# Kernel optimization log

Measured on AMD Instinct MI355X. Metric: run time of the kernel, lower is better.

Reference implementation:

```python
import jax, jax.numpy as jnp
import numpy as np

MAX_LENGTH = 400
NULL_TERM_IND = 52
THR = 1.0 - 1e-05  # F.threshold threshold value


def leaky(x):
    # F.leaky_relu default negative_slope=0.01
    return jnp.where(x >= 0, x, 0.01 * x)


def gru_cell(x, h, w_ih, w_hh, b_ih, b_hh):
    # torch.nn.GRUCell math
    gi = x @ w_ih.T + b_ih          # [B, 3H]
    gh = h @ w_hh.T + b_hh          # [B, 3H]
    i_r, i_z, i_n = jnp.split(gi, 3, axis=-1)
    h_r, h_z, h_n = jnp.split(gh, 3, axis=-1)
    r = jax.nn.sigmoid(i_r + h_r)
    z = jax.nn.sigmoid(i_z + h_z)
    n = jnp.tanh(i_n + r * h_n)
    return (1.0 - z) * n + z * h


def setup_inputs() -> dict:
    key = jax.random.key(0)
    ks = jax.random.split(key, 9)
    B, D, H, C = 2048, 4096, 128, 96
    def init(k, shape, fan):
        return (jax.random.uniform(k, shape, jnp.float32) * 2.0 - 1.0) / np.sqrt(fan)
    return {
        "img_feat": jax.random.normal(ks[0], (B, D), jnp.float32),
        "lin1_w": init(ks[1], (H, D), D),
        "lin1_b": init(ks[2], (H,), D),
        "w_ih": init(ks[3], (3 * H, H), H),
        "w_hh": init(ks[4], (3 * H, H), H),
        "b_ih": init(ks[5], (3 * H,), H),
        "b_hh": init(ks[6], (3 * H,), H),
        "lin2_w": init(ks[7], (C, H), H),
        "lin2_b": init(ks[8], (C,), H),
    }


def reference(img_feat, lin1_w, lin1_b, w_ih, w_hh, b_ih, b_hh, lin2_w, lin2_b):
    # ht: GRU input at t=0 is leaky_relu(lin1(img_feat)); hidden starts at zeros.
    ht = leaky(img_feat @ lin1_w.T + lin1_b)   # [B, 128]
    h0 = jnp.zeros_like(ht)

    def step(carry, _):
        ht, h0 = carry
        hn = gru_cell(ht, h0, w_ih, w_hh, b_ih, b_hh)
        # original: ht = char_gen(ht, h0); h0 = ht -> input == hidden next step
        chars = leaky(hn) @ lin2_w.T + lin2_b   # [B, C]
        m = jax.lax.stop_gradient(jnp.max(chars, axis=-1, keepdims=True))  # .data detach
        cn = chars / m
        cn = jnp.where(cn > THR, cn, 0.0)       # F.threshold(x, 1-1e-5, 0)
        return (hn, hn), cn

    _, titles = jax.lax.scan(step, (ht, h0), None, length=MAX_LENGTH)  # [T, B, C]
    titles = jnp.transpose(titles, (1, 0, 2))   # [B, T, C]

    # title_lens: first t with titles[b, t, NULL_TERM_IND] == 1, else MAX_LENGTH
    eq = titles[:, :, NULL_TERM_IND] == 1.0     # [B, T]
    first = jnp.argmax(eq, axis=1)
    lens = jnp.where(eq.any(axis=1), first + 1, MAX_LENGTH).astype(jnp.int32)
    return titles, lens
```

## Files before the change

### kernel.cpp

```cpp
#include <hip/hip_runtime.h>
#include <math.h>

#define NB   8
#define TT   400
#define HH   128
#define CC   96
#define DD   4096
#define THRV (1.0f - 1e-5f)
#define XR   40
#define HEPS 4e-6f
#define S10  1024.0f
#define IS10 0.0009765625f
#define IS20 9.5367431640625e-07f
#define SCW  132
#define SCS  1056

typedef _Float16 f16x8 __attribute__((ext_vector_type(8)));
typedef float    f32x4 __attribute__((ext_vector_type(4)));
typedef float    f32x2 __attribute__((ext_vector_type(2)));
typedef int      i32x4 __attribute__((ext_vector_type(4)));
typedef unsigned long long ull;

__device__ __forceinline__ float rcp_fast(float x) {
#if __has_builtin(__builtin_amdgcn_rcpf)
    return __builtin_amdgcn_rcpf(x);
#else
    return 1.0f / x;
#endif
}
__device__ __forceinline__ float sigm(float v)  { return rcp_fast(1.0f + __expf(-v)); }
__device__ __forceinline__ float ftanh(float x) { return 1.0f - 2.0f * rcp_fast(1.0f + __expf(2.0f * x)); }

__device__ __forceinline__ void split2(float4 u0, float4 u1, f16x8& hi, f16x8& lo) {
    float x[8] = {u0.x, u0.y, u0.z, u0.w, u1.x, u1.y, u1.z, u1.w};
    #pragma unroll
    for (int e = 0; e < 8; ++e) {
        _Float16 h = (_Float16)x[e];
        hi[e] = h;
        lo[e] = (_Float16)(x[e] - (float)h);
    }
}
__device__ __forceinline__ void split2s(float4 u0, float4 u1, f16x8& hi, f16x8& lo) {
    float x[8] = {u0.x, u0.y, u0.z, u0.w, u1.x, u1.y, u1.z, u1.w};
    #pragma unroll
    for (int e = 0; e < 8; ++e) {
        _Float16 h = (_Float16)x[e];
        hi[e] = h;
        lo[e] = (_Float16)((x[e] - (float)h) * S10);
    }
}
__device__ __forceinline__ void split1(float x, _Float16& hi, _Float16& lo) {
    hi = (_Float16)x;
    lo = (_Float16)(x - (float)hi);
}

__device__ __forceinline__ float xsum32(float v) {
#if __has_builtin(__builtin_amdgcn_permlane32_swap)
    auto r = __builtin_amdgcn_permlane32_swap(__float_as_uint(v), __float_as_uint(v), false, false);
    return __uint_as_float(r[0]) + __uint_as_float(r[1]);
#else
    return v + __shfl_xor(v, 32, 64);
#endif
}

__device__ __forceinline__ void step_barrier() {
    __builtin_amdgcn_sched_barrier(0);
    asm volatile("s_waitcnt lgkmcnt(0)" ::: "memory");
    __builtin_amdgcn_s_barrier();
    asm volatile("" ::: "memory");
    __builtin_amdgcn_sched_barrier(0);
}

__global__ __launch_bounds__(1024, 4)
void gru_title(const float* __restrict__ img,
               const float* __restrict__ l1w,
               const float* __restrict__ l1b,
               const float* __restrict__ wih,
               const float* __restrict__ whh,
               const float* __restrict__ bih,
               const float* __restrict__ bhh,
               const float* __restrict__ l2w,
               const float* __restrict__ l2b,
               float* __restrict__ out,
               float* __restrict__ lens)
{
    __shared__ alignas(16) _Float16 x2 [2][64][XR];
    __shared__ alignas(16) _Float16 l2v[2][64][XR];
    __shared__ alignas(16) char     x2i8[2][64][32];
    __shared__ alignas(16) _Float16 bcS[2][6][4][4][16][8];
    __shared__ alignas(16) float    gEx[4096];
    __shared__ alignas(16) float    scr[2 * SCS];
    __shared__ alignas(16) float    xs0[NB][HH];
    __shared__ int sh_st[4];

    const int tid  = threadIdx.x;
    const int b0   = blockIdx.x * NB;
    const int w    = tid >> 6;
    const int lane = tid & 63;
    const int lm   = lane & 15;
    const int lq   = lane >> 4;
    const int c8   = w & 7;
    const int r8   = w >> 3;
    const int ic2  = 16 * c8 + lm;

    f16x8 bh[2][4];
    i32x4 bq[2][2];
    float gb[2], fq[2];
    #pragma unroll
    for (int gl = 0; gl < 2; ++gl) {
        const int g2 = 2 * r8 + gl;
        const float* r0;
        const float* r1 = nullptr;
        float bsum;
        if (g2 == 0)      { r0 = wih + (size_t)ic2 * HH;         r1 = whh + (size_t)ic2 * HH;         bsum = bih[ic2] + bhh[ic2]; }
        else if (g2 == 1) { r0 = wih + (size_t)(128 + ic2) * HH; r1 = whh + (size_t)(128 + ic2) * HH; bsum = bih[128 + ic2] + bhh[128 + ic2]; }
        else if (g2 == 2) { r0 = wih + (size_t)(256 + ic2) * HH;                                      bsum = bih[256 + ic2]; }
        else              { r0 = whh + (size_t)(256 + ic2) * HH;                                      bsum = bhh[256 + ic2]; }
        gb[gl] = bsum;
        float bl32[4][8];
        #pragma unroll
        for (int kt = 0; kt < 4; ++kt) {
            const int k0 = 32 * kt + 8 * lq;
            float4 u0 = *(const float4*)(r0 + k0);
            float4 u1 = *(const float4*)(r0 + k0 + 4);
            if (r1) {
                float4 e0 = *(const float4*)(r1 + k0);
                float4 e1 = *(const float4*)(r1 + k0 + 4);
                u0.x += e0.x; u0.y += e0.y; u0.z += e0.z; u0.w += e0.w;
                u1.x += e1.x; u1.y += e1.y; u1.z += e1.z; u1.w += e1.w;
            }
            float xv[8] = {u0.x, u0.y, u0.z, u0.w, u1.x, u1.y, u1.z, u1.w};
            f16x8 hiv;
            #pragma unroll
            for (int e = 0; e < 8; ++e) {
                _Float16 hh = (_Float16)xv[e];
                hiv[e] = hh;
                bl32[kt][e] = xv[e] - (float)hh;
            }
            bh[gl][kt] = hiv;
        }
        float mx = 0.f;
        #pragma unroll
        for (int kt = 0; kt < 4; ++kt)
            #pragma unroll
            for (int e = 0; e < 8; ++e) mx = fmaxf(mx, fabsf(bl32[kt][e]));
        mx = fmaxf(mx, __shfl_xor(mx, 16, 64));
        mx = fmaxf(mx, __shfl_xor(mx, 32, 64));
        const float inv = (mx > 0.f) ? 127.0f / mx : 0.f;
        fq[gl] = mx * (1.0f / 16129.0f);
        ull p[4];
        #pragma unroll
        for (int kt = 0; kt < 4; ++kt) {
            ull pv = 0;
            #pragma unroll
            for (int e = 0; e < 8; ++e) {
                int q = (int)rintf(bl32[kt][e] * inv);
                pv |= ((ull)((unsigned)q & 0xffu)) << (8 * e);
            }
            p[kt] = pv;
        }
        #pragma unroll
        for (int ktp = 0; ktp < 2; ++ktp) {
            ull s0a = __shfl(p[2 * ktp],     lm + 16 * ((2 * lq) & 3), 64);
            ull s0b = __shfl(p[2 * ktp + 1], lm + 16 * ((2 * lq) & 3), 64);
            ull lo8 = (lq & 2) ? s0b : s0a;
            ull s1a = __shfl(p[2 * ktp],     lm + 16 * ((2 * lq + 1) & 3), 64);
            ull s1b = __shfl(p[2 * ktp + 1], lm + 16 * ((2 * lq + 1) & 3), 64);
            ull hi8 = (lq & 2) ? s1b : s1a;
            i32x4 f;
            f[0] = (int)(unsigned)(lo8 & 0xffffffffu);
            f[1] = (int)(unsigned)(lo8 >> 32);
            f[2] = (int)(unsigned)(hi8 & 0xffffffffu);
            f[3] = (int)(unsigned)(hi8 >> 32);
            bq[gl][ktp] = f;
        }
    }

    const int ct = (w >= 1 && w <= 6) ? (w - 1) : -1;
    float cb = 0.f;
    if (ct >= 0) cb = l2b[16 * ct + lm];

    for (int idx = tid; idx < 6 * 4 * 4 * 16; idx += 1024) {
        int t_  = idx;
        int lm_ = t_ & 15; t_ >>= 4;
        int lq_ = t_ & 3;  t_ >>= 2;
        int kt_ = t_ & 3;  t_ >>= 2;
        int ct_ = t_;
        const int n  = 16 * ct_ + lm_;
        const int k0 = 32 * kt_ + 8 * lq_;
        #pragma unroll
        for (int e = 0; e < 8; ++e) {
            float v = l2w[(size_t)n * HH + k0 + e];
            _Float16 hi = (_Float16)v;
            bcS[0][ct_][kt_][lq_][lm_][e] = hi;
            bcS[1][ct_][kt_][lq_][lm_][e] = (_Float16)(v - (float)hi);
        }
    }

    if (tid < 4) sh_st[tid] = 1;
    ((int*)x2i8)[tid] = 0;

    {
        const int m8 = lm & 7;
        const float* arow = img + (size_t)(b0 + m8) * DD + 8 * lq + 2048 * r8;
        const float* brow = l1w + (size_t)ic2 * DD + 8 * lq + 2048 * r8;
        f32x4 z4 = {0.f, 0.f, 0.f, 0.f};
        f32x4 accP0 = z4, accP1 = z4, accQ0 = z4, accQ1 = z4;
        auto ptile = [&](int kt, f32x4& aP, f32x4& aQ) {
            float4 a0  = *(const float4*)(arow + 32 * kt);
            float4 a1  = *(const float4*)(arow + 32 * kt + 4);
            float4 bb0 = *(const float4*)(brow + 32 * kt);
            float4 bb1 = *(const float4*)(brow + 32 * kt + 4);
            f16x8 ah, al, bhf, blf;
            split2s(a0, a1, ah, al);
            split2s(bb0, bb1, bhf, blf);
            f16x8 af = (lm >= 8) ? al : ah;
            aP = __builtin_amdgcn_mfma_f32_16x16x32_f16(af, bhf, aP, 0, 0, 0);
            aQ = __builtin_amdgcn_mfma_f32_16x16x32_f16(af, blf, aQ, 0, 0, 0);
        };
        #pragma unroll 2
        for (int kt = 0; kt < 64; kt += 2) {
            ptile(kt,     accP0, accQ0);
            ptile(kt + 1, accP1, accQ1);
        }
        f32x4 P = accP0 + accP1;
        f32x4 Q = accQ0 + accQ1;
        const float sP = (lane < 32) ? 1.0f : IS10;
        const float sQ = (lane < 32) ? IS10 : IS20;
        float s0 = xsum32(P[0] * sP + Q[0] * sQ);
        float s1 = xsum32(P[1] * sP + Q[1] * sQ);
        float s2 = xsum32(P[2] * sP + Q[2] * sQ);
        float s3 = xsum32(P[3] * sP + Q[3] * sQ);
        if (lane < 32) {
            float vv[4] = {s0, s1, s2, s3};
            #pragma unroll
            for (int reg = 0; reg < 4; ++reg)
                scr[r8 * SCS + (4 * lq + reg) * SCW + ic2] = vv[reg];
        }
    }
    __syncthreads();
    {
        const int m = tid >> 7, c = tid & 127;
        float v = scr[m * SCW + c] + scr[SCS + m * SCW + c] + l1b[c];
        xs0[m][c] = (v >= 0.f) ? v : 0.01f * v;
    }
    __syncthreads();

    const int mA = (lane < 32) ? 4 * lq : 4 * (lq - 2) + 2;

    const int mB  = w >> 1;
    const int iB  = 64 * (w & 1) + lane;
    const int kWr = (iB >> 3) & 3;
    const int rBq = 16 * kWr;
    const int cS  = 8 * (((iB >> 5) & 3) ^ kWr) + (iB & 7);
    const int r8q = 16 * ((iB >> 4) & 3) + mB;
    const int c8q = 16 * (iB >> 6) + (iB & 15);
    const unsigned gRd = (unsigned)(mB * 2048 + iB * 16) ^ ((unsigned)(mB & 3) << 5);

    float hreg = 0.f;
    int  len   = TT;
    bool found = false;
    int  tex   = TT;

    auto chars_mfma = [&](int slot, f32x4& cA, f32x4& cB) {
        #pragma unroll
        for (int kt = 0; kt < 4; ++kt) {
            f16x8 cf = *(const f16x8*)&l2v[slot][lane][8 * (kt ^ lq)];
            f16x8 bH = *(const f16x8*)&bcS[0][ct][kt][lq][lm][0];
            f16x8 bL = *(const f16x8*)&bcS[1][ct][kt][lq][lm][0];
            f32x4& a = (kt < 2) ? cA : cB;
            a = __builtin_amdgcn_mfma_f32_16x16x32_f16(cf, bH, a, 0, 0, 0);
            a = __builtin_amdgcn_mfma_f32_16x16x32_f16(cf, bL, a, 0, 0, 0);
        }
    };
    auto chars_commit = [&](int slot, f32x4 cA, f32x4 cB) {
        f32x4 ca = cA + cB;
        const int n = 16 * ct + lm;
        float s0 = xsum32(ca[0]);
        float s1 = xsum32(ca[1]);
        float s2 = xsum32(ca[2]);
        float s3 = xsum32(ca[3]);
        scr[slot * SCS + mA * SCW + n]       = ((lane < 32) ? s0 : s2) + cb;
        scr[slot * SCS + (mA + 1) * SCW + n] = ((lane < 32) ? s1 : s3) + cb;
    };

    auto outrow = [&](int slot, int tme, int r) {
        const float* cr = &scr[slot * SCS + r * SCW];
        float a0 = cr[lane];
        float a1 = cr[32 + lane];
        float a2 = cr[64 + lane];
        float mx = fmaxf(fmaxf(a0, a1), a2);
        mx = fmaxf(mx, __shfl_xor(mx, 16, 32));
        mx = fmaxf(mx, __shfl_xor(mx, 8, 32));
        mx = fmaxf(mx, __shfl_xor(mx, 4, 32));
        mx = fmaxf(mx, __shfl_xor(mx, 2, 32));
        mx = fmaxf(mx, __shfl_xor(mx, 1, 32));
        float q0 = a0 / mx;
        float q1 = a1 / mx;
        float q2 = a2 / mx;
        if (lane < 32) {
            size_t base = ((size_t)(b0 + r) * TT + tme) * CC;
            out[base + lane]      = (q0 > THRV) ? q0 : 0.f;
            out[base + 32 + lane] = (q1 > THRV) ? q1 : 0.f;
            out[base + 64 + lane] = (q2 > THRV) ? q2 : 0.f;
        }
        float q52 = __shfl(q1, 20, 64);
        if (!found && q52 == 1.0f) { found = true; len = tme + 1; }
    };

    for (int t = 0; t < TT; ++t) {
        const int pr = (t + 1) & 1;
        const int pc = t & 1;

        if (t == 0) {
            if (tid < 512) {
                const int g = tid >> 7;
                const int i = tid & 127;
                float bsum;
                if (g == 0)      bsum = bih[i] + bhh[i];
                else if (g == 1) bsum = bih[128 + i] + bhh[128 + i];
                else if (g == 2) bsum = bih[256 + i];
                else             bsum = bhh[256 + i];
                float accT[NB];
                #pragma unroll
                for (int m = 0; m < NB; ++m) accT[m] = bsum;
                if (g < 3) {
                    const float4* wp = (const float4*)(wih + (size_t)(128 * g + i) * HH);
                    #pragma unroll
                    for (int k = 0; k < HH / 4; ++k) {
                        float4 wv = wp[k];
                        #pragma unroll
                        for (int m = 0; m < NB; ++m) {
                            float4 x = *(const float4*)&xs0[m][4 * k];
                            accT[m] += wv.x * x.x + wv.y * x.y + wv.z * x.z + wv.w * x.w;
                        }
                    }
                }
                #pragma unroll
                for (int m = 0; m < NB; ++m) {
                    unsigned off = (unsigned)(m * 2048 + i * 16 + g * 4) ^ ((unsigned)(m & 3) << 5);
                    *(float*)((char*)gEx + off) = accT[m];
                }
            }
        } else {
            f32x4 z4 = {0.f, 0.f, 0.f, 0.f};
            i32x4 iz = {0, 0, 0, 0};
            if (ct >= 0) {
                f32x4 cc0 = z4, cc1 = z4;
                chars_mfma(pr, cc0, cc1);
                chars_commit(pr, cc0, cc1);
            }
            f32x4 acc[2] = {z4, z4};
            i32x4 qac[2] = {iz, iz};
            {
                f16x8 afA = *(const f16x8*)&x2[pr][lane][8 * (0 ^ lq)];
                f16x8 afB = *(const f16x8*)&x2[pr][lane][8 * (1 ^ lq)];
                acc[0] = __builtin_amdgcn_mfma_f32_16x16x32_f16(afA, bh[0][0], acc[0], 0, 0, 0);
                acc[1] = __builtin_amdgcn_mfma_f32_16x16x32_f16(afA, bh[1][0], acc[1], 0, 0, 0);
                acc[0] = __builtin_amdgcn_mfma_f32_16x16x32_f16(afB, bh[0][1], acc[0], 0, 0, 0);
                acc[1] = __builtin_amdgcn_mfma_f32_16x16x32_f16(afB, bh[1][1], acc[1], 0, 0, 0);
                afA = *(const f16x8*)&x2[pr][lane][8 * (2 ^ lq)];
                afB = *(const f16x8*)&x2[pr][lane][8 * (3 ^ lq)];
                acc[0] = __builtin_amdgcn_mfma_f32_16x16x32_f16(afA, bh[0][2], acc[0], 0, 0, 0);
                acc[1] = __builtin_amdgcn_mfma_f32_16x16x32_f16(afA, bh[1][2], acc[1], 0, 0, 0);
                acc[0] = __builtin_amdgcn_mfma_f32_16x16x32_f16(afB, bh[0][3], acc[0], 0, 0, 0);
                acc[1] = __builtin_amdgcn_mfma_f32_16x16x32_f16(afB, bh[1][3], acc[1], 0, 0, 0);
                i32x4 ia = *(const i32x4*)&x2i8[pr][lane][0];
                qac[0] = __builtin_amdgcn_mfma_i32_16x16x64_i8(ia, bq[0][0], qac[0], 0, 0, 0);
                qac[1] = __builtin_amdgcn_mfma_i32_16x16x64_i8(ia, bq[1][0], qac[1], 0, 0, 0);
                ia = *(const i32x4*)&x2i8[pr][lane][16];
                qac[0] = __builtin_amdgcn_mfma_i32_16x16x64_i8(ia, bq[0][1], qac[0], 0, 0, 0);
                qac[1] = __builtin_amdgcn_mfma_i32_16x16x64_i8(ia, bq[1][1], qac[1], 0, 0, 0);
            }
            float G[2][2];
            #pragma unroll
            for (int gl = 0; gl < 2; ++gl) {
                f32x4 t4;
                #pragma unroll
                for (int rr = 0; rr < 4; ++rr)
                    t4[rr] = acc[gl][rr] + fq[gl] * (float)qac[gl][rr];
                float c0 = xsum32(t4[0]);
                float c1 = xsum32(t4[1]);
                float c2 = xsum32(t4[2]);
                float c3 = xsum32(t4[3]);
                G[gl][0] = ((lane < 32) ? c0 : c2) + gb[gl];
                G[gl][1] = ((lane < 32) ? c1 : c3) + gb[gl];
            }
            #pragma unroll
            for (int s = 0; s < 2; ++s) {
                const int m = mA + s;
                unsigned off = (unsigned)(m * 2048 + ic2 * 16 + r8 * 8) ^ ((unsigned)(m & 3) << 5);
                f32x2 v2 = {G[0][s], G[1][s]};
                *(f32x2*)((char*)gEx + off) = v2;
            }
            if (w >= 8 && t >= 2) outrow(pc, t - 2, w - 8);
        }
        step_barrier();

        {
            float4 g4 = *(const float4*)((const char*)gEx + gRd);
            float r = sigm(g4.x);
            float z = sigm(g4.y);
            float n = ftanh(g4.z + r * g4.w);
            float hp = (t == 0) ? 0.f : hreg;
            float h  = (1.f - z) * n + z * hp;
            bool chg = (t < 2) | (fabsf(h - hp) > HEPS);
            hreg = h;
            float lv = (h >= 0.f) ? h : 0.01f * h;
            _Float16 a, b;
            split1(h, a, b);
            x2[pc][rBq + mB][cS]     = a;
            x2[pc][rBq + 8 + mB][cS] = b;
            split1(lv, a, b);
            l2v[pc][rBq + mB][cS]     = a;
            l2v[pc][rBq + 8 + mB][cS] = b;
            x2i8[pc][r8q][c8q] = (char)(int)rintf(h * 127.0f);
            if (chg) sh_st[t & 3] = 0;
        }
        if (tid == 0) sh_st[(t + 2) & 3] = 1;
        step_barrier();
        if (t >= 2 && sh_st[t & 3]) { tex = t; break; }
    }

    if (tex == TT) {
        const int pl = (TT - 1) & 1;
        if (ct >= 0) {
            f32x4 z4 = {0.f, 0.f, 0.f, 0.f};
            f32x4 cc0 = z4, cc1 = z4;
            chars_mfma(pl, cc0, cc1);
            chars_commit(pl, cc0, cc1);
        }
        if (w >= 8) outrow(TT & 1, TT - 2, w - 8);
        __syncthreads();
        if (w >= 8) outrow(pl, TT - 1, w - 8);
    } else if (w >= 8) {
        const int r = w - 8;
        outrow((tex + 1) & 1, tex - 1, r);
        size_t rowbase = (size_t)(b0 + r) * TT * CC;
        #pragma unroll
        for (int p = 0; p < 2; ++p) {
            const float* cr = &scr[p * SCS + r * SCW];
            float a0 = cr[lane];
            float a1 = cr[32 + lane];
            float a2 = cr[64 + lane];
            float mx = fmaxf(fmaxf(a0, a1), a2);
            mx = fmaxf(mx, __shfl_xor(mx, 16, 32));
            mx = fmaxf(mx, __shfl_xor(mx, 8, 32));
            mx = fmaxf(mx, __shfl_xor(mx, 4, 32));
            mx = fmaxf(mx, __shfl_xor(mx, 2, 32));
            mx = fmaxf(mx, __shfl_xor(mx, 1, 32));
            const int u0 = tex + (((tex & 1) == p) ? 0 : 1);
            if (lane < 32) {
                float q0 = a0 / mx;
                float q1 = a1 / mx;
                float q2 = a2 / mx;
                float w0v = (q0 > THRV) ? q0 : 0.f;
                float w1v = (q1 > THRV) ? q1 : 0.f;
                float w2v = (q2 > THRV) ? q2 : 0.f;
                for (int u = u0; u < TT; u += 2) {
                    out[rowbase + (size_t)u * CC + lane]      = w0v;
                    out[rowbase + (size_t)u * CC + 32 + lane] = w1v;
                    out[rowbase + (size_t)u * CC + 64 + lane] = w2v;
                }
            }
        }
    }

    if (w >= 8 && lane == 0) lens[b0 + (w - 8)] = (float)len;
}

extern "C" void kernel_launch(void* const* d_in, const int* in_sizes, int n_in,
                              void* d_out, int out_size, void* d_ws, size_t ws_size,
                              hipStream_t stream)
{
    const float* img = (const float*)d_in[0];
    const float* l1w = (const float*)d_in[1];
    const float* l1b = (const float*)d_in[2];
    const float* wih = (const float*)d_in[3];
    const float* whh = (const float*)d_in[4];
    const float* bih = (const float*)d_in[5];
    const float* bhh = (const float*)d_in[6];
    const float* l2w = (const float*)d_in[7];
    const float* l2b = (const float*)d_in[8];

    float* out  = (float*)d_out;
    float* lens = out + (size_t)2048 * TT * CC;

    gru_title<<<dim3(2048 / NB), dim3(1024), 0, stream>>>(
        img, l1w, l1b, wih, whh, bih, bhh, l2w, l2b, out, lens);
}
```

Before: 587.3 us.

## Remap gate columns so GRU update runs in registers without an LDS exchange barrier

The rows of the gate weight matrices are reassigned so that each wave's MFMA output holds all four gate pre-activations (r, z, n_i, n_h) for the same hidden units, split across lane halves. One shfl_xor swaps them between halves, and each thread then does the GRU update for two batch rows directly in registers. This drops the per-step write of gate values to shared memory, the extra barrier, and the read-back. In exchange, every thread computes two cells, half of those writes are redundant, and lanes diverge on the hi/lo split selects.

```diff
diff --git a/kernel.cpp b/kernel.cpp
--- a/kernel.cpp
+++ b/kernel.cpp
@@ -17,7 +17,6 @@
 
 typedef _Float16 f16x8 __attribute__((ext_vector_type(8)));
 typedef float    f32x4 __attribute__((ext_vector_type(4)));
-typedef float    f32x2 __attribute__((ext_vector_type(2)));
 typedef int      i32x4 __attribute__((ext_vector_type(4)));
 typedef unsigned long long ull;
 
@@ -31,15 +30,6 @@
 __device__ __forceinline__ float sigm(float v)  { return rcp_fast(1.0f + __expf(-v)); }
 __device__ __forceinline__ float ftanh(float x) { return 1.0f - 2.0f * rcp_fast(1.0f + __expf(2.0f * x)); }
 
-__device__ __forceinline__ void split2(float4 u0, float4 u1, f16x8& hi, f16x8& lo) {
-    float x[8] = {u0.x, u0.y, u0.z, u0.w, u1.x, u1.y, u1.z, u1.w};
-    #pragma unroll
-    for (int e = 0; e < 8; ++e) {
-        _Float16 h = (_Float16)x[e];
-        hi[e] = h;
-        lo[e] = (_Float16)(x[e] - (float)h);
-    }
-}
 __device__ __forceinline__ void split2s(float4 u0, float4 u1, f16x8& hi, f16x8& lo) {
     float x[8] = {u0.x, u0.y, u0.z, u0.w, u1.x, u1.y, u1.z, u1.w};
     #pragma unroll
@@ -103,20 +93,27 @@
     const int r8   = w >> 3;
     const int ic2  = 16 * c8 + lm;
 
+    const int  iE  = 8 * w + (lm & 7);
+    const bool hiH = (lm < 8);
     f16x8 bh[2][4];
     i32x4 bq[2][2];
-    float gb[2], fq[2];
+    float gb2[2], fq[2];
     #pragma unroll
-    for (int gl = 0; gl < 2; ++gl) {
-        const int g2 = 2 * r8 + gl;
+    for (int fam = 0; fam < 2; ++fam) {
         const float* r0;
         const float* r1 = nullptr;
         float bsum;
-        if (g2 == 0)      { r0 = wih + (size_t)ic2 * HH;         r1 = whh + (size_t)ic2 * HH;         bsum = bih[ic2] + bhh[ic2]; }
-        else if (g2 == 1) { r0 = wih + (size_t)(128 + ic2) * HH; r1 = whh + (size_t)(128 + ic2) * HH; bsum = bih[128 + ic2] + bhh[128 + ic2]; }
-        else if (g2 == 2) { r0 = wih + (size_t)(256 + ic2) * HH;                                      bsum = bih[256 + ic2]; }
-        else              { r0 = whh + (size_t)(256 + ic2) * HH;                                      bsum = bhh[256 + ic2]; }
-        gb[gl] = bsum;
+        if (fam == 0) {
+            const int row = hiH ? iE : (128 + iE);
+            r0 = wih + (size_t)row * HH;
+            r1 = whh + (size_t)row * HH;
+            bsum = bih[row] + bhh[row];
+        } else {
+            const int row = 256 + iE;
+            r0 = (hiH ? wih : whh) + (size_t)row * HH;
+            bsum = hiH ? bih[row] : bhh[row];
+        }
+        gb2[fam] = bsum;
         float bl32[4][8];
         #pragma unroll
         for (int kt = 0; kt < 4; ++kt) {
@@ -137,7 +134,7 @@
                 hiv[e] = hh;
                 bl32[kt][e] = xv[e] - (float)hh;
             }
-            bh[gl][kt] = hiv;
+            bh[fam][kt] = hiv;
         }
         float mx = 0.f;
         #pragma unroll
@@ -147,7 +144,7 @@
         mx = fmaxf(mx, __shfl_xor(mx, 16, 64));
         mx = fmaxf(mx, __shfl_xor(mx, 32, 64));
         const float inv = (mx > 0.f) ? 127.0f / mx : 0.f;
-        fq[gl] = mx * (1.0f / 16129.0f);
+        fq[fam] = mx * (1.0f / 16129.0f);
         ull p[4];
         #pragma unroll
         for (int kt = 0; kt < 4; ++kt) {
@@ -172,7 +169,7 @@
             f[1] = (int)(unsigned)(lo8 >> 32);
             f[2] = (int)(unsigned)(hi8 & 0xffffffffu);
             f[3] = (int)(unsigned)(hi8 >> 32);
-            bq[gl][ktp] = f;
+            bq[fam][ktp] = f;
         }
     }
 
@@ -248,16 +245,14 @@
 
     const int mA = (lane < 32) ? 4 * lq : 4 * (lq - 2) + 2;
 
-    const int mB  = w >> 1;
-    const int iB  = 64 * (w & 1) + lane;
-    const int kWr = (iB >> 3) & 3;
-    const int rBq = 16 * kWr;
-    const int cS  = 8 * (((iB >> 5) & 3) ^ kWr) + (iB & 7);
-    const int r8q = 16 * ((iB >> 4) & 3) + mB;
-    const int c8q = 16 * (iB >> 6) + (iB & 15);
-    const unsigned gRd = (unsigned)(mB * 2048 + iB * 16) ^ ((unsigned)(mB & 3) << 5);
-
-    float hreg = 0.f;
+    const int kW   = w & 3;
+    const int bs   = ((w >> 2) & 3) ^ kW;
+    const int colf = 8 * bs + (lm & 7);
+    const int rHi  = 16 * kW + (hiH ? 0 : 8);
+    const int r8g  = 16 * ((w >> 1) & 3);
+    const int c8g  = 16 * (w >> 3) + 8 * (w & 1) + (lm & 7);
+
+    float hA = 0.f, hB = 0.f;
     int  len   = TT;
     bool found = false;
     int  tex   = TT;
@@ -311,6 +306,8 @@
     for (int t = 0; t < TT; ++t) {
         const int pr = (t + 1) & 1;
         const int pc = t & 1;
+
+        float R[2], Z[2], NI[2], NH[2];
 
         if (t == 0) {
             if (tid < 512) {
@@ -342,6 +339,14 @@
                     *(float*)((char*)gEx + off) = accT[m];
                 }
             }
+            step_barrier();
+            #pragma unroll
+            for (int s = 0; s < 2; ++s) {
+                const int m = mA + s;
+                unsigned off = (unsigned)(m * 2048 + iE * 16) ^ ((unsigned)(m & 3) << 5);
+                float4 g4 = *(const float4*)((const char*)gEx + off);
+                R[s] = g4.x; Z[s] = g4.y; NI[s] = g4.z; NH[s] = g4.w;
+            }
         } else {
             f32x4 z4 = {0.f, 0.f, 0.f, 0.f};
             i32x4 iz = {0, 0, 0, 0};
@@ -372,51 +377,54 @@
                 qac[0] = __builtin_amdgcn_mfma_i32_16x16x64_i8(ia, bq[0][1], qac[0], 0, 0, 0);
                 qac[1] = __builtin_amdgcn_mfma_i32_16x16x64_i8(ia, bq[1][1], qac[1], 0, 0, 0);
             }
-            float G[2][2];
-            #pragma unroll
-            for (int gl = 0; gl < 2; ++gl) {
+            if (w >= 8 && t >= 2) outrow(pc, t - 2, w - 8);
+            float G2[2][2];
+            #pragma unroll
+            for (int fam = 0; fam < 2; ++fam) {
                 f32x4 t4;
                 #pragma unroll
                 for (int rr = 0; rr < 4; ++rr)
-                    t4[rr] = acc[gl][rr] + fq[gl] * (float)qac[gl][rr];
+                    t4[rr] = acc[fam][rr] + fq[fam] * (float)qac[fam][rr];
                 float c0 = xsum32(t4[0]);
                 float c1 = xsum32(t4[1]);
                 float c2 = xsum32(t4[2]);
                 float c3 = xsum32(t4[3]);
-                G[gl][0] = ((lane < 32) ? c0 : c2) + gb[gl];
-                G[gl][1] = ((lane < 32) ? c1 : c3) + gb[gl];
+                G2[fam][0] = ((lane < 32) ? c0 : c2) + gb2[fam];
+                G2[fam][1] = ((lane < 32) ? c1 : c3) + gb2[fam];
             }
             #pragma unroll
             for (int s = 0; s < 2; ++s) {
-                const int m = mA + s;
-                unsigned off = (unsigned)(m * 2048 + ic2 * 16 + r8 * 8) ^ ((unsigned)(m & 3) << 5);
-                f32x2 v2 = {G[0][s], G[1][s]};
-                *(f32x2*)((char*)gEx + off) = v2;
-            }
-            if (w >= 8 && t >= 2) outrow(pc, t - 2, w - 8);
-        }
-        step_barrier();
-
-        {
-            float4 g4 = *(const float4*)((const char*)gEx + gRd);
-            float r = sigm(g4.x);
-            float z = sigm(g4.y);
-            float n = ftanh(g4.z + r * g4.w);
-            float hp = (t == 0) ? 0.f : hreg;
+                float gx0 = __shfl_xor(G2[0][s], 8, 64);
+                float gx1 = __shfl_xor(G2[1][s], 8, 64);
+                R[s]  = hiH ? G2[0][s] : gx0;
+                Z[s]  = hiH ? gx0      : G2[0][s];
+                NI[s] = hiH ? G2[1][s] : gx1;
+                NH[s] = hiH ? gx1      : G2[1][s];
+            }
+        }
+
+        bool chg = (t < 2);
+        #pragma unroll
+        for (int s = 0; s < 2; ++s) {
+            float hp = (t == 0) ? 0.f : (s ? hB : hA);
+            float r  = sigm(R[s]);
+            float z  = sigm(Z[s]);
+            float n  = ftanh(NI[s] + r * NH[s]);
             float h  = (1.f - z) * n + z * hp;
-            bool chg = (t < 2) | (fabsf(h - hp) > HEPS);
-            hreg = h;
+            chg |= (fabsf(h - hp) > HEPS);
+            if (s) hB = h; else hA = h;
             float lv = (h >= 0.f) ? h : 0.01f * h;
             _Float16 a, b;
             split1(h, a, b);
-            x2[pc][rBq + mB][cS]     = a;
-            x2[pc][rBq + 8 + mB][cS] = b;
+            _Float16 vx = hiH ? a : b;
             split1(lv, a, b);
-            l2v[pc][rBq + mB][cS]     = a;
-            l2v[pc][rBq + 8 + mB][cS] = b;
-            x2i8[pc][r8q][c8q] = (char)(int)rintf(h * 127.0f);
-            if (chg) sh_st[t & 3] = 0;
-        }
+            _Float16 vl = hiH ? a : b;
+            const int row = rHi + mA + s;
+            x2 [pc][row][colf] = vx;
+            l2v[pc][row][colf] = vl;
+            if (hiH) x2i8[pc][r8g + mA + s][c8g] = (char)(int)rintf(h * 127.0f);
+        }
+        if (chg) sh_st[t & 3] = 0;
         if (tid == 0) sh_st[(t + 2) & 3] = 1;
         step_barrier();
         if (t >= 2 && sh_st[t & 3]) { tex = t; break; }
```

New measurement: 599.8 us. 1.02x slower.
